# Optimization experiments

Hardware: AMD Instinct MI355X
Metric: run time of the kernel (lower is better)

The kernel has to match this reference:

```python
import jax, jax.numpy as jnp
import numpy as np

B, T = 64, 1000
Q_DIM, M_DIM, A_DIM = 1024, 512, 128
N_FILT, KSIZE = 32, 31
PAD = (KSIZE - 1) // 2


def setup_inputs() -> dict:
    key = jax.random.key(0)
    ks = jax.random.split(key, 12)
    inp = {
        "query": jax.random.normal(ks[0], (B, Q_DIM), dtype=jnp.float32),
        "memory": jax.random.normal(ks[1], (B, T, M_DIM), dtype=jnp.float32),
        "attention_weights_cum": jax.random.uniform(ks[2], (B, 1, T), dtype=jnp.float32),
        "mask": jnp.zeros((B, T), dtype=bool),
        # params (Linear weights stored [out, in] like torch)
        "Wq": jax.random.normal(ks[3], (A_DIM, Q_DIM), dtype=jnp.float32) * 0.03,
        "bq": jnp.zeros((A_DIM,), dtype=jnp.float32),
        "Wm": jax.random.normal(ks[4], (A_DIM, M_DIM), dtype=jnp.float32) * 0.04,
        "bm": jnp.zeros((A_DIM,), dtype=jnp.float32),
        "Wv": jax.random.normal(ks[5], (1, A_DIM), dtype=jnp.float32) * 0.09,
        "bv": jnp.zeros((1,), dtype=jnp.float32),
        "conv_w": jax.random.normal(ks[6], (N_FILT, 1, KSIZE), dtype=jnp.float32) * 0.18,
        "conv_b": jnp.zeros((N_FILT,), dtype=jnp.float32),
        "Wloc": jax.random.normal(ks[7], (A_DIM, N_FILT), dtype=jnp.float32) * 0.18,
    }
    return inp


def reference(query, memory, attention_weights_cum, mask,
              Wq, bq, Wm, bm, Wv, bv, conv_w, conv_b, Wloc):
    # key projection: [B, T, A]
    key = jnp.einsum('btm,am->bta', memory, Wm) + bm
    # query projection: [B, 1, A]
    q = (query @ Wq.T + bq)[:, None, :]
    # location conv: [B,1,T] -> [B,N_FILT,T]
    loc = jax.lax.conv_general_dilated(
        attention_weights_cum, conv_w, window_strides=(1,),
        padding=[(PAD, PAD)], dimension_numbers=('NCH', 'OIH', 'NCH'))
    loc = loc + conv_b[None, :, None]
    # [B, T, A]
    loc = jnp.einsum('bft,af->bta', loc, Wloc)
    # energies: [B, T]
    energies = (jnp.tanh(q + loc + key) @ Wv.T + bv)[..., 0]
    alignment = jnp.where(mask, -jnp.inf, energies)
    attention_weights = jax.nn.softmax(alignment, axis=1)  # [B, T]
    attention_context = jnp.einsum('bt,btm->bm', attention_weights, memory)
    return attention_context, attention_weights
```

## Files before the change

kernel.cpp:

```cpp
#include <hip/hip_runtime.h>
#include <math.h>

#define Bsz 64
#define Tn 1000
#define QD 1024
#define MD 512
#define AD 128
#define NF 32
#define KS 31
#define PADc 15

#define NCH 16
#define RPC 64
#define SUB 16
#define ROWSH 520

typedef __attribute__((ext_vector_type(8))) short bf16x8;
typedef __attribute__((ext_vector_type(4))) float f32x4;

#define OFF_ENERG 32768
#define OFF_WMF  288768
#define OFF_W2F  419840
#define OFF_ML   428032
#define OFF_CTXC 436224

static __device__ __forceinline__ short f2bf(float x) {
    unsigned u = __float_as_uint(x);
    unsigned r = (u + 0x7fffu + ((u >> 16) & 1u)) >> 16;
    return (short)r;
}
static __device__ __forceinline__ float bf2f(short s) {
    return __uint_as_float(((unsigned)(unsigned short)s) << 16);
}
static __device__ __forceinline__ float fast_tanh(float x) {
    float e2 = __expf(2.f * x);
    return 1.f - 2.f / (e2 + 1.f);
}

__global__ __launch_bounds__(256)
void k_prep(const float* __restrict__ Wm, const float* __restrict__ conv_w,
            const float* __restrict__ conv_b, const float* __restrict__ Wloc,
            const float* __restrict__ query, const float* __restrict__ Wq,
            const float* __restrict__ bq, const float* __restrict__ bm,
            short* __restrict__ WmF, short* __restrict__ W2F,
            float* __restrict__ qsum) {
    __shared__ float qs[QD];
    __shared__ float red[256];
    int bid = blockIdx.x;
    if (bid < 32) {
        int g = bid * 256 + threadIdx.x;
        int wc = g >> 6, l = g & 63;
        int a = (wc >> 4) * 16 + (l & 15);
        int kb = (wc & 15) * 32 + (l >> 4) * 8;
        const float* src = Wm + a * MD + kb;
        float4 v0 = *(const float4*)src;
        float4 v1 = *(const float4*)(src + 4);
        bf16x8 o;
        o[0] = f2bf(v0.x); o[1] = f2bf(v0.y); o[2] = f2bf(v0.z); o[3] = f2bf(v0.w);
        o[4] = f2bf(v1.x); o[5] = f2bf(v1.y); o[6] = f2bf(v1.z); o[7] = f2bf(v1.w);
        *(bf16x8*)(WmF + (size_t)g * 8) = o;
    } else if (bid < 96) {
        int b = bid - 32;
        int a = threadIdx.x & 127;
        int half = threadIdx.x >> 7;
        for (int i = threadIdx.x; i < QD; i += 256) qs[i] = query[b * QD + i];
        __syncthreads();
        const float4* Wq4 = (const float4*)(Wq + a * QD + half * (QD / 2));
        const float4* qs4 = (const float4*)(qs + half * (QD / 2));
        float acc = 0.f;
#pragma unroll 4
        for (int i = 0; i < QD / 8; ++i) {
            float4 w = Wq4[i];
            float4 q = qs4[i];
            acc += w.x * q.x + w.y * q.y + w.z * q.z + w.w * q.w;
        }
        red[threadIdx.x] = acc;
        __syncthreads();
        if (half == 0) {
            float b2 = 0.f;
            for (int f = 0; f < NF; ++f) b2 += conv_b[f] * Wloc[a * NF + f];
            qsum[b * AD + a] = red[a] + red[a + 128] + bq[a] + bm[a] + b2;
        }
    } else {
        for (int s = threadIdx.x * 2; s < threadIdx.x * 2 + 2; ++s) {
            int w = s >> 6, l = s & 63;
            int a = w * 16 + (l & 15);
            int kb = (l >> 4) * 8;
            bf16x8 o;
#pragma unroll
            for (int j = 0; j < 8; ++j) {
                int k = kb + j;
                float sum = 0.f;
                if (k < KS)
                    for (int f = 0; f < NF; ++f) sum += conv_w[f * KS + k] * Wloc[a * NF + f];
                o[j] = f2bf(sum);
            }
            *(bf16x8*)(W2F + s * 8) = o;
        }
    }
}

__global__ __launch_bounds__(512, 4)
void k_fused(const float* __restrict__ mem, const float* __restrict__ awc,
             const unsigned char* __restrict__ mask,
             const short* __restrict__ WmF, const short* __restrict__ W2F,
             const float* __restrict__ Wv, const float* __restrict__ bv,
             const float* __restrict__ qsum, float* __restrict__ energ,
             float* __restrict__ ctxc, float2* __restrict__ ml) {
    __shared__ __align__(16) short chunk[RPC * ROWSH];
    __shared__ float ered[8][SUB + 1];
    __shared__ float Esub[RPC];
    __shared__ float ps[RPC];
    __shared__ float vmask[RPC];
    __shared__ short awcsB[96];

    const int b = blockIdx.y, c = blockIdx.x;
    const int t0 = c * RPC;
    const int tid = threadIdx.x;
    const int w = tid >> 6, lane = tid & 63, m16 = lane & 15, q = lane >> 4;

    bf16x8 bf[17];
#pragma unroll
    for (int cc = 0; cc < 16; ++cc) bf[cc] = ((const bf16x8*)WmF)[(w * 16 + cc) * 64 + lane];
    bf[16] = ((const bf16x8*)W2F)[w * 64 + lane];

    const int a = w * 16 + m16;
    const float wvv = Wv[a];
    const float qsv = qsum[b * AD + a];
    const float bv0 = bv[0];

    if (tid < 96) {
        int g = t0 - PADc + tid;
        float v = (tid <= 94 && g >= 0 && g < Tn) ? awc[b * Tn + g] : 0.f;
        awcsB[tid] = f2bf(v);
    }
    if (tid < RPC) {
        int t = t0 + tid;
        bool valid = (t < Tn) && (mask[b * Tn + (t < Tn ? t : 0)] == 0);
        vmask[tid] = valid ? 1.f : 0.f;
    }

    const float* gbase = mem + (size_t)b * Tn * MD + lane * 8;
    float4 stg[2][2][2];
#pragma unroll
    for (int rr = 0; rr < 2; ++rr) {
        int t = t0 + w * 2 + rr;
        int tc = t < Tn ? t : Tn - 1;
        const float* p = gbase + (size_t)tc * MD;
        stg[0][rr][0] = *(const float4*)p;
        stg[0][rr][1] = *(const float4*)(p + 4);
    }

    asm volatile("s_waitcnt lgkmcnt(0)" ::: "memory");
    __builtin_amdgcn_s_barrier();

#pragma unroll
    for (int s = 0; s < 4; ++s) {
#pragma unroll
        for (int rr = 0; rr < 2; ++rr) {
            int row = s * SUB + w * 2 + rr;
            float4 v0 = stg[s & 1][rr][0];
            float4 v1 = stg[s & 1][rr][1];
            bf16x8 o;
            o[0] = f2bf(v0.x); o[1] = f2bf(v0.y); o[2] = f2bf(v0.z); o[3] = f2bf(v0.w);
            o[4] = f2bf(v1.x); o[5] = f2bf(v1.y); o[6] = f2bf(v1.z); o[7] = f2bf(v1.w);
            *(bf16x8*)(&chunk[row * ROWSH] + lane * 8) = o;
        }
        if (s < 3) {
#pragma unroll
            for (int rr = 0; rr < 2; ++rr) {
                int t = t0 + (s + 1) * SUB + w * 2 + rr;
                int tc = t < Tn ? t : Tn - 1;
                const float* p = gbase + (size_t)tc * MD;
                stg[(s + 1) & 1][rr][0] = *(const float4*)p;
                stg[(s + 1) & 1][rr][1] = *(const float4*)(p + 4);
            }
        }
        asm volatile("s_waitcnt lgkmcnt(0)" ::: "memory");
        __builtin_amdgcn_s_barrier();

        f32x4 acc = (f32x4){0.f, 0.f, 0.f, 0.f};
        const short* arow = &chunk[(s * SUB + m16) * ROWSH + q * 8];
#pragma unroll
        for (int cc = 0; cc < 16; ++cc) {
            bf16x8 af = *(const bf16x8*)(arow + cc * 32);
            acc = __builtin_amdgcn_mfma_f32_16x16x32_bf16(af, bf[cc], acc, 0, 0, 0);
        }
        {
            int tl = s * SUB + m16;
            bf16x8 af;
#pragma unroll
            for (int j = 0; j < 8; ++j) af[j] = awcsB[tl + q * 8 + j];
            acc = __builtin_amdgcn_mfma_f32_16x16x32_bf16(af, bf[16], acc, 0, 0, 0);
        }

#pragma unroll
        for (int r = 0; r < 4; ++r) {
            float e = wvv * fast_tanh(acc[r] + qsv);
#pragma unroll
            for (int m2 = 1; m2 < 16; m2 <<= 1) e += __shfl_xor(e, m2, 64);
            if (m16 == 0) ered[w][q * 4 + r] = e;
        }
        asm volatile("s_waitcnt lgkmcnt(0)" ::: "memory");
        __builtin_amdgcn_s_barrier();
        if (tid < SUB) {
            float E = bv0;
#pragma unroll
            for (int ww = 0; ww < 8; ++ww) E += ered[ww][tid];
            Esub[s * SUB + tid] = E;
        }
    }

    asm volatile("s_waitcnt lgkmcnt(0)" ::: "memory");
    __builtin_amdgcn_s_barrier();

    float mx = -1e30f;
#pragma unroll
    for (int r = 0; r < RPC; ++r) {
        float e = (vmask[r] != 0.f) ? Esub[r] : -1e30f;
        mx = fmaxf(mx, e);
    }
    if (tid < RPC) ps[tid] = vmask[tid] * __expf(Esub[tid] - mx);
    asm volatile("s_waitcnt lgkmcnt(0)" ::: "memory");
    __builtin_amdgcn_s_barrier();

    float ctxj = 0.f, psum = 0.f;
#pragma unroll 8
    for (int r = 0; r < RPC; ++r) {
        float p = ps[r];
        psum += p;
        ctxj += p * bf2f(chunk[r * ROWSH + tid]);
    }
    ctxc[((size_t)c * Bsz + b) * MD + tid] = ctxj;
    if (tid < RPC) {
        int t = t0 + tid;
        if (t < Tn) energ[b * Tn + t] = Esub[tid];
    }
    if (tid == 0) ml[c * Bsz + b] = make_float2(mx, psum);
}

__global__ __launch_bounds__(512)
void k_combine(const float* __restrict__ ctxc, const float2* __restrict__ ml,
               const float* __restrict__ energ, const unsigned char* __restrict__ mask,
               float* __restrict__ ctx, float* __restrict__ wout) {
    __shared__ float sm[NCH], sl[NCH];
    int b = blockIdx.x;
    int tid = threadIdx.x;
    if (tid < NCH) {
        float2 v = ml[tid * Bsz + b];
        sm[tid] = v.x;
        sl[tid] = v.y;
    }
    __syncthreads();
    float M = -1e30f;
#pragma unroll
    for (int cc = 0; cc < NCH; ++cc) M = fmaxf(M, sm[cc]);
    float L = 0.f;
#pragma unroll
    for (int cc = 0; cc < NCH; ++cc) L += sl[cc] * __expf(sm[cc] - M);
    float inv = 1.f / L;

    float s = 0.f;
#pragma unroll
    for (int cc = 0; cc < NCH; ++cc)
        s += ctxc[((size_t)cc * Bsz + b) * MD + tid] * __expf(sm[cc] - M);
    ctx[b * MD + tid] = s * inv;

#pragma unroll
    for (int i = 0; i < 2; ++i) {
        int t = tid + i * 512;
        if (t < Tn) {
            bool msk = mask[b * Tn + t] != 0;
            float e = energ[b * Tn + t];
            wout[b * Tn + t] = msk ? 0.f : __expf(e - M) * inv;
        }
    }
}

extern "C" void kernel_launch(void* const* d_in, const int* in_sizes, int n_in,
                              void* d_out, int out_size, void* d_ws, size_t ws_size,
                              hipStream_t stream) {
    const float* query  = (const float*)d_in[0];
    const float* memory = (const float*)d_in[1];
    const float* awc    = (const float*)d_in[2];
    const unsigned char* mask = (const unsigned char*)d_in[3];
    const float* Wq     = (const float*)d_in[4];
    const float* bq     = (const float*)d_in[5];
    const float* Wm     = (const float*)d_in[6];
    const float* bm     = (const float*)d_in[7];
    const float* Wv     = (const float*)d_in[8];
    const float* bv     = (const float*)d_in[9];
    const float* conv_w = (const float*)d_in[10];
    const float* conv_b = (const float*)d_in[11];
    const float* Wloc   = (const float*)d_in[12];

    float* out = (float*)d_out;
    float* ctx = out;
    float* wout = out + Bsz * MD;

    float* qsum  = (float*)d_ws;
    float* energ = (float*)((char*)d_ws + OFF_ENERG);
    short* WmF   = (short*)((char*)d_ws + OFF_WMF);
    short* W2F   = (short*)((char*)d_ws + OFF_W2F);
    float2* ml   = (float2*)((char*)d_ws + OFF_ML);
    float* ctxc  = (float*)((char*)d_ws + OFF_CTXC);

    k_prep<<<dim3(97), dim3(256), 0, stream>>>(Wm, conv_w, conv_b, Wloc, query, Wq,
                                               bq, bm, WmF, W2F, qsum);
    k_fused<<<dim3(NCH, Bsz), dim3(512), 0, stream>>>(
        memory, awc, mask, WmF, W2F, Wv, bv, qsum, energ, ctxc, ml);
    k_combine<<<dim3(Bsz), dim3(512), 0, stream>>>(ctxc, ml, energ, mask, ctx, wout);
}
```

Baseline: 245.4 us.

## Stream memory through double-buffered LDS with online softmax, two chunks per block

The fused kernel now keeps only two 16-row bf16 buffers in LDS instead of the whole 64-row chunk, and folds the context accumulation into an online-softmax update after each 16-row sub-tile. Each block handles 128 timesteps and emits two partial chunks, so half as many blocks are launched and the per-block weight fragment loads are amortised. The smaller LDS footprint is meant to allow more resident blocks. In exchange there are extra barriers and exp rescaling per sub-tile, and fewer total blocks to spread across the CUs.

```diff
diff --git a/kernel.cpp b/kernel.cpp
--- a/kernel.cpp
+++ b/kernel.cpp
@@ -62,11 +62,11 @@
     } else if (bid < 96) {
         int b = bid - 32;
         int a = threadIdx.x & 127;
-        int half = threadIdx.x >> 7;
+        int half_ = threadIdx.x >> 7;
         for (int i = threadIdx.x; i < QD; i += 256) qs[i] = query[b * QD + i];
         __syncthreads();
-        const float4* Wq4 = (const float4*)(Wq + a * QD + half * (QD / 2));
-        const float4* qs4 = (const float4*)(qs + half * (QD / 2));
+        const float4* Wq4 = (const float4*)(Wq + a * QD + half_ * (QD / 2));
+        const float4* qs4 = (const float4*)(qs + half_ * (QD / 2));
         float acc = 0.f;
 #pragma unroll 4
         for (int i = 0; i < QD / 8; ++i) {
@@ -76,7 +76,7 @@
         }
         red[threadIdx.x] = acc;
         __syncthreads();
-        if (half == 0) {
+        if (half_ == 0) {
             float b2 = 0.f;
             for (int f = 0; f < NF; ++f) b2 += conv_b[f] * Wloc[a * NF + f];
             qsum[b * AD + a] = red[a] + red[a + 128] + bq[a] + bm[a] + b2;
@@ -107,136 +107,144 @@
              const float* __restrict__ Wv, const float* __restrict__ bv,
              const float* __restrict__ qsum, float* __restrict__ energ,
              float* __restrict__ ctxc, float2* __restrict__ ml) {
-    __shared__ __align__(16) short chunk[RPC * ROWSH];
+    __shared__ __align__(16) short buf[2][SUB * ROWSH];
     __shared__ float ered[8][SUB + 1];
-    __shared__ float Esub[RPC];
-    __shared__ float ps[RPC];
-    __shared__ float vmask[RPC];
-    __shared__ short awcsB[96];
-
-    const int b = blockIdx.y, c = blockIdx.x;
-    const int t0 = c * RPC;
+    __shared__ __align__(16) float Em[SUB];
+    __shared__ float vm[2 * RPC];
+    __shared__ short awcsB[160];
+
+    const int b = blockIdx.y, c2 = blockIdx.x;
+    const int t0 = c2 * (2 * RPC);
     const int tid = threadIdx.x;
     const int w = tid >> 6, lane = tid & 63, m16 = lane & 15, q = lane >> 4;
 
-    bf16x8 bf[17];
-#pragma unroll
-    for (int cc = 0; cc < 16; ++cc) bf[cc] = ((const bf16x8*)WmF)[(w * 16 + cc) * 64 + lane];
-    bf[16] = ((const bf16x8*)W2F)[w * 64 + lane];
+    const float* gbase = mem + (size_t)b * Tn * MD + lane * 8;
+    float4 stg[2][2][2];
+#pragma unroll
+    for (int rr = 0; rr < 2; ++rr) {
+        int t = t0 + w * 2 + rr;
+        int tc = t < Tn ? t : Tn - 1;
+        const float* gp = gbase + (size_t)tc * MD;
+        stg[0][rr][0] = *(const float4*)gp;
+        stg[0][rr][1] = *(const float4*)(gp + 4);
+    }
+
+    if (tid < 160) {
+        int g = t0 - PADc + tid;
+        float v = (tid <= 158 && g >= 0 && g < Tn) ? awc[b * Tn + g] : 0.f;
+        awcsB[tid] = f2bf(v);
+    }
+    if (tid < 2 * RPC) {
+        int t = t0 + tid;
+        vm[tid] = (t < Tn && mask[b * Tn + t] == 0) ? 1.f : 0.f;
+    }
+
+    bf16x8 bfr[17];
+#pragma unroll
+    for (int cc = 0; cc < 16; ++cc) bfr[cc] = ((const bf16x8*)WmF)[(w * 16 + cc) * 64 + lane];
+    bfr[16] = ((const bf16x8*)W2F)[w * 64 + lane];
 
     const int a = w * 16 + m16;
     const float wvv = Wv[a];
     const float qsv = qsum[b * AD + a];
     const float bv0 = bv[0];
 
-    if (tid < 96) {
-        int g = t0 - PADc + tid;
-        float v = (tid <= 94 && g >= 0 && g < Tn) ? awc[b * Tn + g] : 0.f;
-        awcsB[tid] = f2bf(v);
-    }
-    if (tid < RPC) {
-        int t = t0 + tid;
-        bool valid = (t < Tn) && (mask[b * Tn + (t < Tn ? t : 0)] == 0);
-        vmask[tid] = valid ? 1.f : 0.f;
-    }
-
-    const float* gbase = mem + (size_t)b * Tn * MD + lane * 8;
-    float4 stg[2][2][2];
-#pragma unroll
-    for (int rr = 0; rr < 2; ++rr) {
-        int t = t0 + w * 2 + rr;
-        int tc = t < Tn ? t : Tn - 1;
-        const float* p = gbase + (size_t)tc * MD;
-        stg[0][rr][0] = *(const float4*)p;
-        stg[0][rr][1] = *(const float4*)(p + 4);
-    }
-
     asm volatile("s_waitcnt lgkmcnt(0)" ::: "memory");
     __builtin_amdgcn_s_barrier();
 
-#pragma unroll
-    for (int s = 0; s < 4; ++s) {
-#pragma unroll
-        for (int rr = 0; rr < 2; ++rr) {
-            int row = s * SUB + w * 2 + rr;
-            float4 v0 = stg[s & 1][rr][0];
-            float4 v1 = stg[s & 1][rr][1];
-            bf16x8 o;
-            o[0] = f2bf(v0.x); o[1] = f2bf(v0.y); o[2] = f2bf(v0.z); o[3] = f2bf(v0.w);
-            o[4] = f2bf(v1.x); o[5] = f2bf(v1.y); o[6] = f2bf(v1.z); o[7] = f2bf(v1.w);
-            *(bf16x8*)(&chunk[row * ROWSH] + lane * 8) = o;
-        }
-        if (s < 3) {
+    float mrun = -1e30f, lrun = 0.f, ctxj = 0.f;
+
+#pragma unroll
+    for (int hf = 0; hf < 2; ++hf) {
+#pragma unroll
+        for (int sl = 0; sl < 4; ++sl) {
+            const int ss = hf * 4 + sl;
+            const int pb = ss & 1;
 #pragma unroll
             for (int rr = 0; rr < 2; ++rr) {
-                int t = t0 + (s + 1) * SUB + w * 2 + rr;
-                int tc = t < Tn ? t : Tn - 1;
-                const float* p = gbase + (size_t)tc * MD;
-                stg[(s + 1) & 1][rr][0] = *(const float4*)p;
-                stg[(s + 1) & 1][rr][1] = *(const float4*)(p + 4);
-            }
-        }
-        asm volatile("s_waitcnt lgkmcnt(0)" ::: "memory");
-        __builtin_amdgcn_s_barrier();
-
-        f32x4 acc = (f32x4){0.f, 0.f, 0.f, 0.f};
-        const short* arow = &chunk[(s * SUB + m16) * ROWSH + q * 8];
-#pragma unroll
-        for (int cc = 0; cc < 16; ++cc) {
-            bf16x8 af = *(const bf16x8*)(arow + cc * 32);
-            acc = __builtin_amdgcn_mfma_f32_16x16x32_bf16(af, bf[cc], acc, 0, 0, 0);
-        }
-        {
-            int tl = s * SUB + m16;
-            bf16x8 af;
-#pragma unroll
-            for (int j = 0; j < 8; ++j) af[j] = awcsB[tl + q * 8 + j];
-            acc = __builtin_amdgcn_mfma_f32_16x16x32_bf16(af, bf[16], acc, 0, 0, 0);
-        }
-
-#pragma unroll
-        for (int r = 0; r < 4; ++r) {
-            float e = wvv * fast_tanh(acc[r] + qsv);
-#pragma unroll
-            for (int m2 = 1; m2 < 16; m2 <<= 1) e += __shfl_xor(e, m2, 64);
-            if (m16 == 0) ered[w][q * 4 + r] = e;
-        }
-        asm volatile("s_waitcnt lgkmcnt(0)" ::: "memory");
-        __builtin_amdgcn_s_barrier();
-        if (tid < SUB) {
-            float E = bv0;
-#pragma unroll
-            for (int ww = 0; ww < 8; ++ww) E += ered[ww][tid];
-            Esub[s * SUB + tid] = E;
-        }
-    }
-
-    asm volatile("s_waitcnt lgkmcnt(0)" ::: "memory");
-    __builtin_amdgcn_s_barrier();
-
-    float mx = -1e30f;
-#pragma unroll
-    for (int r = 0; r < RPC; ++r) {
-        float e = (vmask[r] != 0.f) ? Esub[r] : -1e30f;
-        mx = fmaxf(mx, e);
-    }
-    if (tid < RPC) ps[tid] = vmask[tid] * __expf(Esub[tid] - mx);
-    asm volatile("s_waitcnt lgkmcnt(0)" ::: "memory");
-    __builtin_amdgcn_s_barrier();
-
-    float ctxj = 0.f, psum = 0.f;
-#pragma unroll 8
-    for (int r = 0; r < RPC; ++r) {
-        float p = ps[r];
-        psum += p;
-        ctxj += p * bf2f(chunk[r * ROWSH + tid]);
-    }
-    ctxc[((size_t)c * Bsz + b) * MD + tid] = ctxj;
-    if (tid < RPC) {
-        int t = t0 + tid;
-        if (t < Tn) energ[b * Tn + t] = Esub[tid];
-    }
-    if (tid == 0) ml[c * Bsz + b] = make_float2(mx, psum);
+                int row = w * 2 + rr;
+                float4 v0 = stg[pb][rr][0];
+                float4 v1 = stg[pb][rr][1];
+                bf16x8 o;
+                o[0] = f2bf(v0.x); o[1] = f2bf(v0.y); o[2] = f2bf(v0.z); o[3] = f2bf(v0.w);
+                o[4] = f2bf(v1.x); o[5] = f2bf(v1.y); o[6] = f2bf(v1.z); o[7] = f2bf(v1.w);
+                *(bf16x8*)(&buf[pb][row * ROWSH] + lane * 8) = o;
+            }
+            if (ss < 7) {
+#pragma unroll
+                for (int rr = 0; rr < 2; ++rr) {
+                    int t = t0 + (ss + 1) * SUB + w * 2 + rr;
+                    int tc = t < Tn ? t : Tn - 1;
+                    const float* gp = gbase + (size_t)tc * MD;
+                    stg[pb ^ 1][rr][0] = *(const float4*)gp;
+                    stg[pb ^ 1][rr][1] = *(const float4*)(gp + 4);
+                }
+            }
+            asm volatile("s_waitcnt lgkmcnt(0)" ::: "memory");
+            __builtin_amdgcn_s_barrier();
+
+            f32x4 acc = (f32x4){0.f, 0.f, 0.f, 0.f};
+            const short* arow = &buf[pb][m16 * ROWSH + q * 8];
+#pragma unroll
+            for (int cc = 0; cc < 16; ++cc) {
+                bf16x8 af = *(const bf16x8*)(arow + cc * 32);
+                acc = __builtin_amdgcn_mfma_f32_16x16x32_bf16(af, bfr[cc], acc, 0, 0, 0);
+            }
+            {
+                int tl = ss * SUB + m16;
+                bf16x8 af;
+#pragma unroll
+                for (int j = 0; j < 8; ++j) af[j] = awcsB[tl + q * 8 + j];
+                acc = __builtin_amdgcn_mfma_f32_16x16x32_bf16(af, bfr[16], acc, 0, 0, 0);
+            }
+
+#pragma unroll
+            for (int r = 0; r < 4; ++r) {
+                float e = wvv * fast_tanh(acc[r] + qsv);
+#pragma unroll
+                for (int m2 = 1; m2 < 16; m2 <<= 1) e += __shfl_xor(e, m2, 64);
+                if (m16 == 0) ered[w][q * 4 + r] = e;
+            }
+            asm volatile("s_waitcnt lgkmcnt(0)" ::: "memory");
+            __builtin_amdgcn_s_barrier();
+            if (tid < SUB) {
+                float E = bv0;
+#pragma unroll
+                for (int ww = 0; ww < 8; ++ww) E += ered[ww][tid];
+                int t = t0 + ss * SUB + tid;
+                if (t < Tn) energ[b * Tn + t] = E;
+                Em[tid] = (vm[ss * SUB + tid] != 0.f) ? E : -1e30f;
+            }
+            asm volatile("s_waitcnt lgkmcnt(0)" ::: "memory");
+            __builtin_amdgcn_s_barrier();
+
+            float es[16];
+            *(float4*)&es[0]  = *(const float4*)&Em[0];
+            *(float4*)&es[4]  = *(const float4*)&Em[4];
+            *(float4*)&es[8]  = *(const float4*)&Em[8];
+            *(float4*)&es[12] = *(const float4*)&Em[12];
+            float msub = es[0];
+#pragma unroll
+            for (int r = 1; r < 16; ++r) msub = fmaxf(msub, es[r]);
+            float mnew = fmaxf(mrun, msub);
+            float sc = __expf(mrun - mnew);
+            lrun *= sc;
+            ctxj *= sc;
+            mrun = mnew;
+            if (mnew > -5e29f) {
+#pragma unroll
+                for (int r = 0; r < 16; ++r) {
+                    float pr = __expf(es[r] - mnew);
+                    lrun += pr;
+                    ctxj += pr * bf2f(buf[pb][r * ROWSH + tid]);
+                }
+            }
+        }
+        int c = 2 * c2 + hf;
+        ctxc[((size_t)c * Bsz + b) * MD + tid] = ctxj;
+        if (tid == 0) ml[c * Bsz + b] = make_float2(mrun, lrun);
+        mrun = -1e30f; lrun = 0.f; ctxj = 0.f;
+    }
 }
 
 __global__ __launch_bounds__(512)
@@ -307,7 +315,7 @@
 
     k_prep<<<dim3(97), dim3(256), 0, stream>>>(Wm, conv_w, conv_b, Wloc, query, Wq,
                                                bq, bm, WmF, W2F, qsum);
-    k_fused<<<dim3(NCH, Bsz), dim3(512), 0, stream>>>(
+    k_fused<<<dim3(NCH / 2, Bsz), dim3(512), 0, stream>>>(
         memory, awc, mask, WmF, W2F, Wv, bv, qsum, energ, ctxc, ml);
     k_combine<<<dim3(Bsz), dim3(512), 0, stream>>>(ctxc, ml, energ, mask, ctx, wout);
 }
```

Measured after the change: 250.5 us. +2.1%, slower.
